# Kernel tuning notes

Measured on AMD Instinct MI355X. Metric: run time of the kernel, lower is better.

Reference implementation:

```python
import jax, jax.numpy as jnp
import numpy as np
from jax import lax

C = 64
KS = 3  # filter_ks for dynamic kernel conv


def conv2d(x, w, pad, b=None):
    out = lax.conv_general_dilated(x, w, (1, 1), [(pad, pad), (pad, pad)],
                                   dimension_numbers=("NCHW", "OIHW", "NCHW"))
    if b is not None:
        out = out + b.reshape(1, -1, 1, 1)
    return out


def kernel_conv2d(feat, kernel):
    # feat: [B,C,H,W]; kernel: [B,C*KS*KS,H,W] -> per-pixel per-channel 3x3 filter
    B, Cc, H, W = feat.shape
    pad = (KS - 1) // 2
    xp = jnp.pad(feat, ((0, 0), (0, 0), (pad, pad), (pad, pad)), mode="edge")
    # patches: [B,C,KS*KS,H,W]
    patches = jnp.stack([xp[:, :, i:i + H, j:j + W]
                         for i in range(KS) for j in range(KS)], axis=2)
    K = kernel.reshape(B, Cc, KS * KS, H, W)
    return jnp.sum(patches * K, axis=2)


def setup_inputs() -> dict:
    key = jax.random.key(0)
    ks = jax.random.split(key, 24)
    B, H, W = 8, 128, 128
    s = lambda *sh: 1.0 / np.sqrt(np.prod(sh[1:]))
    def w(k, *sh):
        return jax.random.normal(k, sh, dtype=jnp.float32) * s(*sh)
    return {
        "f_event": jax.random.normal(ks[0], (B, C, H, W), dtype=jnp.float32),
        "f_blur": jax.random.normal(ks[1], (B, C, H, W), dtype=jnp.float32),
        # trans: conv3x3 -> ReLU -> conv3x3 (no bias)
        "Wt1": w(ks[2], C, C, 3, 3), "Wt2": w(ks[3], C, C, 3, 3),
        # trans2: conv3x3 -> ReLU
        "Wt3": w(ks[4], C, C, 3, 3),
        # F_mlp: Linear(C,2C) -> ReLU -> Linear(2C,C) -> Sigmoid
        "A1": w(ks[5], 2 * C, C), "b1": jnp.zeros((2 * C,), jnp.float32),
        "A2": w(ks[6], C, 2 * C), "b2": jnp.zeros((C,), jnp.float32),
        # gernerate_kernel: conv3x3(bias) -> ReLU -> conv1x1(bias) to C*KS^2
        "G1": w(ks[7], C, C, 3, 3), "g1b": jnp.zeros((C,), jnp.float32),
        "G2": w(ks[8], C * KS * KS, C, 1, 1), "g2b": jnp.zeros((C * KS * KS,), jnp.float32),
        # gate_rgb: conv1x1 C->1, bias
        "Rw": w(ks[9], 1, C, 1, 1), "rb": jnp.zeros((1,), jnp.float32),
        # body_sa: conv3x3 -> ReLU -> conv3x3 (no bias)
        "S1": w(ks[10], C, C, 3, 3), "S2": w(ks[11], C, C, 3, 3),
        # spatial_e: BasicConv(2,1,5,pad=2,relu=False), bias
        "Ew": w(ks[12], 1, 2, 5, 5), "eb": jnp.zeros((1,), jnp.float32),
        # conv1x1_fusion: 2C->2C, no bias
        "Fw": w(ks[13], 2 * C, 2 * C, 1, 1),
    }


def reference(f_event, f_blur, Wt1, Wt2, Wt3, A1, b1, A2, b2,
              G1, g1b, G2, g2b, Rw, rb, S1, S2, Ew, eb, Fw):
    fused = f_event + f_blur
    fused = conv2d(jax.nn.relu(conv2d(fused, Wt1, 1)), Wt2, 1)  # trans
    # SE-style channel gate
    w0 = jnp.mean(fused, axis=(2, 3))                      # [B,C]
    w0 = jax.nn.relu(w0 @ A1.T + b1)
    w0 = jax.nn.sigmoid(w0 @ A2.T + b2)                    # [B,C]
    f_b = f_blur + w0[:, :, None, None] * f_blur
    fused2 = fused + jax.nn.relu(conv2d(fused, Wt3, 1))    # trans2 + residual
    rgb_att = conv2d(fused2, Rw, 0, rb)                    # [B,1,H,W]
    f_b = f_b + rgb_att * f_b
    # dynamic per-pixel kernel from events
    kern = conv2d(jax.nn.relu(conv2d(f_event, G1, 1, g1b)), G2, 0, g2b)
    f_b = f_b + kernel_conv2d(f_b, kern)
    # spatial attention on events
    sa = conv2d(jax.nn.relu(conv2d(f_event, S1, 1)), S2, 1)
    comp = jnp.concatenate([jnp.max(sa, axis=1, keepdims=True),
                            jnp.mean(sa, axis=1, keepdims=True)], axis=1)
    scale_e = jax.nn.sigmoid(conv2d(comp, Ew, 2, eb))      # [B,1,H,W]
    f_e = f_event + scale_e * f_event
    res = conv2d(jnp.concatenate([f_e, f_b], axis=1), Fw, 0)
    return res
```

## Files before the change

kernel.cpp:

```cpp
#include <hip/hip_runtime.h>
#include <math.h>

constexpr int Bn = 8, Cn = 64, Hn = 128, Wn = 128;
constexpr int HW  = Hn * Wn;
constexpr int CHW = Cn * HW;
constexpr size_t NB = (size_t)Bn * CHW;

typedef float  f32x4  __attribute__((ext_vector_type(4)));
typedef __bf16 bf16x8 __attribute__((ext_vector_type(8)));
typedef unsigned int u32x4 __attribute__((ext_vector_type(4)));
typedef unsigned int u32x2 __attribute__((ext_vector_type(2)));

static __device__ __forceinline__ unsigned short f2bf(float f) {
    unsigned u = __builtin_bit_cast(unsigned, f);
    u = (u + 0x7FFF + ((u >> 16) & 1)) >> 16;
    return (unsigned short)u;
}
static __device__ __forceinline__ float bf2f(unsigned short v) {
    unsigned u = (unsigned)v << 16;
    return __builtin_bit_cast(float, u);
}
static __device__ __forceinline__ float bfhalf(unsigned u, int hi) {
    unsigned r = hi ? (u & 0xffff0000u) : (u << 16);
    return __builtin_bit_cast(float, r);
}

static __device__ __forceinline__ void gl_lds16(const unsigned short* g, unsigned short* l) {
#if defined(__has_builtin) && __has_builtin(__builtin_amdgcn_global_load_lds)
    __builtin_amdgcn_global_load_lds(
        (const __attribute__((address_space(1))) void*)g,
        (__attribute__((address_space(3))) void*)l, 16, 0, 0);
#else
    *(u32x4*)l = *(const u32x4*)g;
#endif
}

__global__ void prep_w_k(const float* __restrict__ W0, const float* __restrict__ W1,
                         const float* __restrict__ W2, const float* __restrict__ W3,
                         const float* __restrict__ W4, const float* __restrict__ W5,
                         unsigned short* __restrict__ dst) {
    int i = blockIdx.x * 256 + threadIdx.x;
    if (i >= 36864) return;
    const float* W = W0;
    switch (blockIdx.y) {
        case 1: W = W1; break; case 2: W = W2; break;
        case 3: W = W3; break; case 4: W = W4; break; case 5: W = W5; break;
        default: break;
    }
    int cj = i & 7;
    int rest = i >> 3;
    int co = rest & 63;
    rest >>= 6;
    int t  = rest % 9;
    int hs = rest / 9;
    int ci = hs * 8 + cj;
    dst[(size_t)blockIdx.y * 36864 + i] = f2bf(W[(co * 64 + ci) * 9 + t]);
}

__global__ void prep2_k(const float* __restrict__ G2, const float* __restrict__ Fw,
                        unsigned short* __restrict__ G2p, unsigned short* __restrict__ Fwp,
                        unsigned short* __restrict__ zp) {
    int i = blockIdx.x * 256 + threadIdx.x;
    if (i < 64) zp[i] = 0;
    if (i < 36864) G2p[i] = f2bf(G2[i]);
    else if (i < 36864 + 16384) Fwp[i - 36864] = f2bf(Fw[i - 36864]);
}

__global__ void pre_blk_k(const float* __restrict__ fe, const float* __restrict__ fb,
                          unsigned short* __restrict__ evb, unsigned short* __restrict__ f0b,
                          unsigned short* __restrict__ fbb) {
    int i = blockIdx.x * 256 + threadIdx.x;
    int px = i & 16383;
    int oct = (i >> 14) & 7;
    int b = i >> 17;
    const float* pe = fe + (size_t)b * CHW + (size_t)oct * 8 * HW + px;
    const float* pb = fb + (size_t)b * CHW + (size_t)oct * 8 * HW + px;
    u32x4 ev, f0, fbv;
#pragma unroll
    for (int q = 0; q < 4; ++q) {
        float e0 = pe[(size_t)(2 * q) * HW],     b0 = pb[(size_t)(2 * q) * HW];
        float e1 = pe[(size_t)(2 * q + 1) * HW], b1 = pb[(size_t)(2 * q + 1) * HW];
        ev[q]  = (unsigned)f2bf(e0) | ((unsigned)f2bf(e1) << 16);
        f0[q]  = (unsigned)f2bf(e0 + b0) | ((unsigned)f2bf(e1 + b1) << 16);
        fbv[q] = (unsigned)f2bf(b0) | ((unsigned)f2bf(b1) << 16);
    }
    const size_t o = ((size_t)(b * 8 + oct) * HW + px) * 8;
    *(u32x4*)(evb + o) = ev;
    *(u32x4*)(f0b + o) = f0;
    *(u32x4*)(fbb + o) = fbv;
}

__global__ __launch_bounds__(256, 3) void conv3x3_l1_blk(
        const unsigned short* __restrict__ f0, const unsigned short* __restrict__ ev,
        const unsigned short* __restrict__ Wt1g, const unsigned short* __restrict__ G1g,
        const unsigned short* __restrict__ S1g, const float* __restrict__ g1b,
        unsigned short* __restrict__ out_t1, unsigned short* __restrict__ out_h,
        unsigned short* __restrict__ out_s1, const unsigned short* __restrict__ zp) {
    __shared__ unsigned short smIn[20736];
    const int z = blockIdx.z;
    const int b = z & 7, sel = z >> 3;
    const unsigned short* in = (sel == 0) ? f0 : ev;
    const unsigned short* Wg = (sel == 0) ? Wt1g : ((sel == 1) ? G1g : S1g);
    unsigned short* out = (sel == 0) ? out_t1 : ((sel == 1) ? out_h : out_s1);
    const int by = blockIdx.y << 4, bx = blockIdx.x << 4;
    const int tid = threadIdx.x;
    const int lane = tid & 63, w = tid >> 6;
    const int lx = lane & 15, ls = lane >> 4;

    for (int idx = tid; idx < 2592; idx += 256) {
        int oct = idx / 324;
        int p   = idx - oct * 324;
        int yy = p / 18, xx = p - yy * 18;
        int gy = by + yy - 1, gx = bx + xx - 1;
        const unsigned short* src =
            ((unsigned)gy < (unsigned)Hn && (unsigned)gx < (unsigned)Wn)
            ? in + ((size_t)(b * 8 + oct) * HW + gy * Wn + gx) * 8 : zp;
        gl_lds16(src, smIn + idx * 8);
    }
    __syncthreads();

    f32x4 acc[4][4];
#pragma unroll
    for (int m = 0; m < 4; ++m)
#pragma unroll
        for (int n = 0; n < 4; ++n) acc[m][n] = f32x4{0.f, 0.f, 0.f, 0.f};

#pragma unroll
    for (int ky = 0; ky < 3; ++ky)
#pragma unroll
    for (int kx = 0; kx < 3; ++kx) {
        const int t = ky * 3 + kx;
#pragma unroll
        for (int kk = 0; kk < 2; ++kk) {
            bf16x8 a[4];
            const unsigned short* wbase = Wg + kk * 18432 + ls * 4608 + t * 512 + lx * 8;
#pragma unroll
            for (int m = 0; m < 4; ++m)
                a[m] = *(const bf16x8*)(wbase + m * 128);
            const unsigned short* ibase =
                smIn + ((kk * 4 + ls) * 324 + (4 * w + ky) * 18 + lx + kx) * 8;
#pragma unroll
            for (int n = 0; n < 4; ++n) {
                bf16x8 bf = *(const bf16x8*)(ibase + n * 144);
#pragma unroll
                for (int m = 0; m < 4; ++m)
                    acc[m][n] = __builtin_amdgcn_mfma_f32_16x16x32_bf16(
                        a[m], bf, acc[m][n], 0, 0, 0);
            }
        }
    }

    const int y0 = by + 4 * w;
#pragma unroll
    for (int m = 0; m < 4; ++m) {
        float bv[4] = {0.f, 0.f, 0.f, 0.f};
        if (sel == 1) {
            float4 b4 = *(const float4*)(g1b + 16 * m + ls * 4);
            bv[0] = b4.x; bv[1] = b4.y; bv[2] = b4.z; bv[3] = b4.w;
        }
        const size_t rowb = (size_t)(b * 8 + m * 2 + (ls >> 1)) * HW;
        const int j0 = (ls & 1) * 4;
#pragma unroll
        for (int n = 0; n < 4; ++n) {
            const size_t pofs = rowb + (size_t)(y0 + n) * Wn + bx + lx;
            float vr[4];
#pragma unroll
            for (int r = 0; r < 4; ++r)
                vr[r] = fmaxf(acc[m][n][r] + bv[r], 0.f);
            u32x2 pk;
            pk[0] = (unsigned)f2bf(vr[0]) | ((unsigned)f2bf(vr[1]) << 16);
            pk[1] = (unsigned)f2bf(vr[2]) | ((unsigned)f2bf(vr[3]) << 16);
            *(u32x2*)(out + pofs * 8 + j0) = pk;
        }
    }
}

__global__ __launch_bounds__(256, 3) void conv3x3_l2_blk(
        const unsigned short* __restrict__ t1, const unsigned short* __restrict__ s1,
        const unsigned short* __restrict__ Wt2g, const unsigned short* __restrict__ S2g,
        unsigned short* __restrict__ out_f, float* __restrict__ comp,
        const unsigned short* __restrict__ zp) {
    __shared__ unsigned short smIn[20736];
    const int z = blockIdx.z;
    const int b = z & 7, sel = z >> 3;
    const unsigned short* in = (sel == 0) ? t1 : s1;
    const unsigned short* Wg = (sel == 0) ? Wt2g : S2g;
    const int by = blockIdx.y << 4, bx = blockIdx.x << 4;
    const int tid = threadIdx.x;
    const int lane = tid & 63, w = tid >> 6;
    const int lx = lane & 15, ls = lane >> 4;

    for (int idx = tid; idx < 2592; idx += 256) {
        int oct = idx / 324;
        int p   = idx - oct * 324;
        int yy = p / 18, xx = p - yy * 18;
        int gy = by + yy - 1, gx = bx + xx - 1;
        const unsigned short* src =
            ((unsigned)gy < (unsigned)Hn && (unsigned)gx < (unsigned)Wn)
            ? in + ((size_t)(b * 8 + oct) * HW + gy * Wn + gx) * 8 : zp;
        gl_lds16(src, smIn + idx * 8);
    }
    __syncthreads();

    f32x4 acc[4][4];
#pragma unroll
    for (int m = 0; m < 4; ++m)
#pragma unroll
        for (int n = 0; n < 4; ++n) acc[m][n] = f32x4{0.f, 0.f, 0.f, 0.f};

#pragma unroll
    for (int ky = 0; ky < 3; ++ky)
#pragma unroll
    for (int kx = 0; kx < 3; ++kx) {
        const int t = ky * 3 + kx;
#pragma unroll
        for (int kk = 0; kk < 2; ++kk) {
            bf16x8 a[4];
            const unsigned short* wbase = Wg + kk * 18432 + ls * 4608 + t * 512 + lx * 8;
#pragma unroll
            for (int m = 0; m < 4; ++m)
                a[m] = *(const bf16x8*)(wbase + m * 128);
            const unsigned short* ibase =
                smIn + ((kk * 4 + ls) * 324 + (4 * w + ky) * 18 + lx + kx) * 8;
#pragma unroll
            for (int n = 0; n < 4; ++n) {
                bf16x8 bf = *(const bf16x8*)(ibase + n * 144);
#pragma unroll
                for (int m = 0; m < 4; ++m)
                    acc[m][n] = __builtin_amdgcn_mfma_f32_16x16x32_bf16(
                        a[m], bf, acc[m][n], 0, 0, 0);
            }
        }
    }

    const int y0 = by + 4 * w;
    if (sel == 0) {
#pragma unroll
        for (int m = 0; m < 4; ++m) {
            const size_t rowb = (size_t)(b * 8 + m * 2 + (ls >> 1)) * HW;
            const int j0 = (ls & 1) * 4;
#pragma unroll
            for (int n = 0; n < 4; ++n) {
                const size_t pofs = rowb + (size_t)(y0 + n) * Wn + bx + lx;
                u32x2 pk;
                pk[0] = (unsigned)f2bf(acc[m][n][0]) | ((unsigned)f2bf(acc[m][n][1]) << 16);
                pk[1] = (unsigned)f2bf(acc[m][n][2]) | ((unsigned)f2bf(acc[m][n][3]) << 16);
                *(u32x2*)(out_f + pofs * 8 + j0) = pk;
            }
        }
    } else {
        float gs[4], gm[4];
#pragma unroll
        for (int n = 0; n < 4; ++n) { gs[n] = 0.f; gm[n] = -1e30f; }
#pragma unroll
        for (int m = 0; m < 4; ++m)
#pragma unroll
            for (int r = 0; r < 4; ++r)
#pragma unroll
                for (int n = 0; n < 4; ++n) {
                    float v = acc[m][n][r];
                    gm[n] = fmaxf(gm[n], v);
                    gs[n] += v;
                }
#pragma unroll
        for (int n = 0; n < 4; ++n) {
            float s = gs[n], mx = gm[n];
            s += __shfl_xor(s, 16);
            s += __shfl_xor(s, 32);
            mx = fmaxf(mx, __shfl_xor(mx, 16));
            mx = fmaxf(mx, __shfl_xor(mx, 32));
            if (ls == 0) {
                const size_t o = (size_t)b * 2 * HW + (size_t)(y0 + n) * Wn + bx + lx;
                comp[o]      = mx;
                comp[o + HW] = s * (1.f / 64.f);
            }
        }
    }
}

__global__ __launch_bounds__(256, 3) void rgb_sconv_k(
        const unsigned short* __restrict__ in, const unsigned short* __restrict__ Wg,
        const float* __restrict__ gw, const float* __restrict__ gb,
        float* __restrict__ gout,
        const float* __restrict__ comp, const float* __restrict__ Ew,
        const float* __restrict__ eb, float* __restrict__ scale,
        const unsigned short* __restrict__ zp) {
    __shared__ unsigned short smIn[20736];
    const int z = blockIdx.z;
    if (z >= 8) {
        int id = (((z - 8) * 64) + blockIdx.y * 8 + blockIdx.x) * 256 + threadIdx.x;
        int sb = id >> 14, p = id & 16383;
        int y = p >> 7, x = p & 127;
        const float* cb = comp + (size_t)sb * 2 * HW;
        float sacc = eb[0];
#pragma unroll
        for (int ch = 0; ch < 2; ++ch)
#pragma unroll
            for (int ky = 0; ky < 5; ++ky) {
                int gy = y + ky - 2;
                if ((unsigned)gy >= (unsigned)Hn) continue;
#pragma unroll
                for (int kx = 0; kx < 5; ++kx) {
                    int gx = x + kx - 2;
                    if ((unsigned)gx >= (unsigned)Wn) continue;
                    sacc = fmaf(Ew[ch * 25 + ky * 5 + kx], cb[ch * HW + gy * Wn + gx], sacc);
                }
            }
        scale[id] = 1.f / (1.f + expf(-sacc));
        return;
    }
    const int b = z;
    const int by = blockIdx.y << 4, bx = blockIdx.x << 4;
    const int tid = threadIdx.x;
    const int lane = tid & 63, w = tid >> 6;
    const int lx = lane & 15, ls = lane >> 4;

    for (int idx = tid; idx < 2592; idx += 256) {
        int oct = idx / 324;
        int p   = idx - oct * 324;
        int yy = p / 18, xx = p - yy * 18;
        int gy = by + yy - 1, gx = bx + xx - 1;
        const unsigned short* src =
            ((unsigned)gy < (unsigned)Hn && (unsigned)gx < (unsigned)Wn)
            ? in + ((size_t)(b * 8 + oct) * HW + gy * Wn + gx) * 8 : zp;
        gl_lds16(src, smIn + idx * 8);
    }
    __syncthreads();

    f32x4 acc[4][4];
#pragma unroll
    for (int m = 0; m < 4; ++m)
#pragma unroll
        for (int n = 0; n < 4; ++n) acc[m][n] = f32x4{0.f, 0.f, 0.f, 0.f};

#pragma unroll
    for (int ky = 0; ky < 3; ++ky)
#pragma unroll
    for (int kx = 0; kx < 3; ++kx) {
        const int t = ky * 3 + kx;
#pragma unroll
        for (int kk = 0; kk < 2; ++kk) {
            bf16x8 a[4];
            const unsigned short* wbase = Wg + kk * 18432 + ls * 4608 + t * 512 + lx * 8;
#pragma unroll
            for (int m = 0; m < 4; ++m)
                a[m] = *(const bf16x8*)(wbase + m * 128);
            const unsigned short* ibase =
                smIn + ((kk * 4 + ls) * 324 + (4 * w + ky) * 18 + lx + kx) * 8;
#pragma unroll
            for (int n = 0; n < 4; ++n) {
                bf16x8 bf = *(const bf16x8*)(ibase + n * 144);
#pragma unroll
                for (int m = 0; m < 4; ++m)
                    acc[m][n] = __builtin_amdgcn_mfma_f32_16x16x32_bf16(
                        a[m], bf, acc[m][n], 0, 0, 0);
            }
        }
    }

    const int y0 = by + 4 * w;
    float gs[4];
#pragma unroll
    for (int n = 0; n < 4; ++n) gs[n] = 0.f;
#pragma unroll
    for (int m = 0; m < 4; ++m) {
        float4 rw4 = *(const float4*)(gw + 16 * m + ls * 4);
        const float rwf[4] = {rw4.x, rw4.y, rw4.z, rw4.w};
        const size_t rowb = (size_t)(b * 8 + m * 2 + (ls >> 1)) * HW;
        const int j0 = (ls & 1) * 4;
#pragma unroll
        for (int n = 0; n < 4; ++n) {
            const size_t pofs = rowb + (size_t)(y0 + n) * Wn + bx + lx;
            u32x2 rin = *(const u32x2*)(in + pofs * 8 + j0);
#pragma unroll
            for (int r = 0; r < 4; ++r) {
                float v = fmaxf(acc[m][n][r], 0.f) + bfhalf(rin[r >> 1], r & 1);
                gs[n] = fmaf(rwf[r], v, gs[n]);
            }
        }
    }
#pragma unroll
    for (int n = 0; n < 4; ++n) {
        float s = gs[n];
        s += __shfl_xor(s, 16);
        s += __shfl_xor(s, 32);
        if (ls == 0)
            gout[(size_t)b * HW + (size_t)(y0 + n) * Wn + bx + lx] = s + gb[0];
    }
}

__global__ void mean_hw_blk(const unsigned short* __restrict__ in, float* __restrict__ w0) {
    __shared__ float red[256][8];
    const int bo = blockIdx.x;
    const int tid = threadIdx.x;
    const unsigned short* p = in + (size_t)bo * HW * 8;
    float s[8];
#pragma unroll
    for (int j = 0; j < 8; ++j) s[j] = 0.f;
    for (int it = 0; it < 64; ++it) {
        u32x4 v = *(const u32x4*)(p + (size_t)(tid + it * 256) * 8);
#pragma unroll
        for (int j = 0; j < 8; ++j) s[j] += bfhalf(v[j >> 1], j & 1);
    }
#pragma unroll
    for (int j = 0; j < 8; ++j) red[tid][j] = s[j];
    __syncthreads();
    for (int off = 128; off > 0; off >>= 1) {
        if (tid < off)
#pragma unroll
            for (int j = 0; j < 8; ++j) red[tid][j] += red[tid + off][j];
        __syncthreads();
    }
    if (tid < 8) w0[bo * 8 + tid] = red[0][tid] * (1.f / 16384.f);
}

__global__ void mlp_k(const float* __restrict__ w0, const float* __restrict__ A1,
                      const float* __restrict__ b1, const float* __restrict__ A2,
                      const float* __restrict__ b2, float* __restrict__ w0s) {
    int b = blockIdx.x, t = threadIdx.x;
    __shared__ float w0r[64], hid[128];
    if (t < 64) w0r[t] = w0[b * 64 + t];
    __syncthreads();
    float s = b1[t];
    for (int c = 0; c < 64; ++c) s = fmaf(A1[t * 64 + c], w0r[c], s);
    hid[t] = fmaxf(s, 0.f);
    __syncthreads();
    if (t < 64) {
        float s2 = b2[t];
        for (int j = 0; j < 128; ++j) s2 = fmaf(A2[t * 128 + j], hid[j], s2);
        w0s[b * 64 + t] = 1.f / (1.f + expf(-s2));
    }
}

__global__ __launch_bounds__(256, 4) void dynfused_k(
        const unsigned short* __restrict__ fbb, const unsigned short* __restrict__ hb,
        const unsigned short* __restrict__ G2p, const float* __restrict__ g2b,
        const float* __restrict__ w0s, const float* __restrict__ rgb,
        unsigned short* __restrict__ outb) {
    __shared__ unsigned short smU[8192];
    __shared__ unsigned short smFB[11520];
    const int b  = blockIdx.z;
    const int by = blockIdx.y << 3, bx = blockIdx.x << 4;
    const int tid = threadIdx.x;
    const int lane = tid & 63, w = tid >> 6;
    const int lx = lane & 15, ls = lane >> 4;
    const int wr = w & 1, wc = w >> 1;
    const int px = tid & 127;
    const int chalf = __builtin_amdgcn_readfirstlane(tid >> 7);
    const int ty = px >> 4, tx = px & 15;

#pragma unroll
    for (int it = 0; it < 4; ++it) {
        int i = tid + it * 256;
        int p = i & 127, oct = i >> 7;
        gl_lds16(hb + ((size_t)(b * 8 + oct) * HW + (by + (p >> 4)) * Wn + bx + (p & 15)) * 8,
                 smU + i * 8);
    }
    const float* rgbb = rgb + (size_t)b * HW;
    for (int i = tid; i < 1440; i += 256) {
        int oct = i / 180, p = i - oct * 180;
        int pr = p / 18, pc = p - pr * 18;
        int gy = min(max(by + pr - 1, 0), Hn - 1);
        int gx = min(max(bx + pc - 1, 0), Wn - 1);
        u32x4 v = *(const u32x4*)(fbb + ((size_t)(b * 8 + oct) * HW + gy * Wn + gx) * 8);
        float g = 1.f + rgbb[gy * Wn + gx];
        float4 s0 = *(const float4*)(w0s + b * 64 + oct * 8);
        float4 s1 = *(const float4*)(w0s + b * 64 + oct * 8 + 4);
        const float sc[8] = {1.f + s0.x, 1.f + s0.y, 1.f + s0.z, 1.f + s0.w,
                             1.f + s1.x, 1.f + s1.y, 1.f + s1.z, 1.f + s1.w};
#pragma unroll
        for (int j = 0; j < 8; ++j)
            smFB[(oct * 8 + j) * 180 + p] = f2bf(bfhalf(v[j >> 1], j & 1) * sc[j] * g);
    }
    __syncthreads();

    bf16x8 bv[2][4];
#pragma unroll
    for (int kk = 0; kk < 2; ++kk)
#pragma unroll
        for (int n = 0; n < 4; ++n)
            bv[kk][n] = *(const bf16x8*)(smU + ((kk * 4 + ls) * 128 + wc * 64 + n * 16 + lx) * 8);
    __syncthreads();

    float acc[32];
#pragma unroll
    for (int s = 0; s < 32; ++s) acc[s] = 0.f;

#pragma unroll
    for (int chunk = 0; chunk < 9; ++chunk) {
        f32x4 ka[2][4];
#pragma unroll
        for (int m = 0; m < 2; ++m)
#pragma unroll
            for (int n = 0; n < 4; ++n) ka[m][n] = f32x4{0.f, 0.f, 0.f, 0.f};
#pragma unroll
        for (int kk = 0; kk < 2; ++kk) {
            bf16x8 a[2];
#pragma unroll
            for (int m = 0; m < 2; ++m)
                a[m] = *(const bf16x8*)(G2p +
                        (size_t)(chunk * 64 + wr * 32 + m * 16 + lx) * 64 + kk * 32 + ls * 8);
#pragma unroll
            for (int n = 0; n < 4; ++n)
#pragma unroll
                for (int m = 0; m < 2; ++m)
                    ka[m][n] = __builtin_amdgcn_mfma_f32_16x16x32_bf16(a[m], bv[kk][n], ka[m][n], 0, 0, 0);
        }
#pragma unroll
        for (int m = 0; m < 2; ++m) {
            const float4 bb4 = *(const float4*)(g2b + chunk * 64 + wr * 32 + m * 16 + ls * 4);
            const float bb[4] = {bb4.x, bb4.y, bb4.z, bb4.w};
            const int rl0 = wr * 32 + m * 16 + ls * 4;
            const int gr = rl0 >> 3, sub = rl0 & 7;
#pragma unroll
            for (int n = 0; n < 4; ++n) {
                const int pxl = wc * 64 + n * 16 + lx;
                u32x2 pk;
                pk[0] = (unsigned)f2bf(ka[m][n][0] + bb[0]) |
                        ((unsigned)f2bf(ka[m][n][1] + bb[1]) << 16);
                pk[1] = (unsigned)f2bf(ka[m][n][2] + bb[2]) |
                        ((unsigned)f2bf(ka[m][n][3] + bb[3]) << 16);
                *(u32x2*)(smU + pxl * 64 + ((gr ^ (pxl & 7)) << 3) + sub) = pk;
            }
        }
        __syncthreads();
        u32x4 kvr[8];
#pragma unroll
        for (int k = 0; k < 8; ++k)
            kvr[k] = *(const u32x4*)(smU + px * 64 + ((k ^ (px & 7)) << 3));
#pragma unroll
        for (int rl = 0; rl < 64; ++rl) {
            const int r = chunk * 64 + rl;
            const int c = r / 9, t = r - c * 9;
            const int s = c >> 1;
            if ((c & 1) == chalf) {
                float kv = bfhalf(kvr[rl >> 3][(rl & 7) >> 1], rl & 1);
                float pv = bf2f(smFB[c * 180 + (ty + t / 3) * 18 + tx + (t % 3)]);
                acc[s] = fmaf(kv, pv, acc[s]);
            }
        }
        __syncthreads();
    }

#pragma unroll
    for (int s = 0; s < 32; ++s) {
        const int c = 2 * s + chalf;
        float res = bf2f(smFB[c * 180 + (ty + 1) * 18 + (tx + 1)]);
        smU[c * 128 + px] = f2bf(acc[s] + res);
    }
    __syncthreads();
#pragma unroll
    for (int it = 0; it < 4; ++it) {
        int i = tid + it * 256;
        int p = i & 127, oct = i >> 7;
        u32x4 pk;
#pragma unroll
        for (int q = 0; q < 4; ++q)
            pk[q] = (unsigned)smU[(oct * 8 + 2 * q) * 128 + p] |
                    ((unsigned)smU[(oct * 8 + 2 * q + 1) * 128 + p] << 16);
        *(u32x4*)(outb + ((size_t)(b * 8 + oct) * HW + (by + (p >> 4)) * Wn + bx + (p & 15)) * 8) = pk;
    }
}

__global__ __launch_bounds__(256, 3) void fuse_mfma_k(
        const unsigned short* __restrict__ evb, const float* __restrict__ scale,
        const unsigned short* __restrict__ fb2b, const unsigned short* __restrict__ Fwp,
        float* __restrict__ out) {
    __shared__ unsigned short smF[16384];
    const int bid = blockIdx.x;
    const int b = bid >> 7, px0 = (bid & 127) << 7;
    const int tid = threadIdx.x;
    const int lane = tid & 63, w = tid >> 6;
    const int lx = lane & 15, ls = lane >> 4;
    const int wr = w & 1, wc = w >> 1;
    const float* sc = scale + b * HW + px0;

#pragma unroll
    for (int it = 4; it < 8; ++it) {
        int slot = tid + it * 256;
        int oct = slot >> 7, pxl = slot & 127;
        gl_lds16(fb2b + ((size_t)(b * 8 + oct - 8) * HW + px0 + pxl) * 8, smF + slot * 8);
    }
#pragma unroll
    for (int it = 0; it < 4; ++it) {
        int slot = tid + it * 256;
        int oct = slot >> 7, pxl = slot & 127;
        u32x4 v = *(const u32x4*)(evb + ((size_t)(b * 8 + oct) * HW + px0 + pxl) * 8);
        float s = 1.f + sc[pxl];
#pragma unroll
        for (int q = 0; q < 4; ++q)
            v[q] = (unsigned)f2bf(bfhalf(v[q], 0) * s) |
                   ((unsigned)f2bf(bfhalf(v[q], 1) * s) << 16);
        ((u32x4*)smF)[slot] = v;
    }
    __syncthreads();

    f32x4 acc[4][4];
#pragma unroll
    for (int m = 0; m < 4; ++m)
#pragma unroll
        for (int n = 0; n < 4; ++n) acc[m][n] = f32x4{0.f, 0.f, 0.f, 0.f};

#pragma unroll
    for (int kk = 0; kk < 4; ++kk) {
        bf16x8 a[4];
#pragma unroll
        for (int m = 0; m < 4; ++m)
            a[m] = *(const bf16x8*)(Fwp + (size_t)(wr * 64 + m * 16 + lx) * 128 + kk * 32 + ls * 8);
#pragma unroll
        for (int n = 0; n < 4; ++n) {
            bf16x8 bv = *(const bf16x8*)(smF + ((kk * 4 + ls) * 128 + wc * 64 + n * 16 + lx) * 8);
#pragma unroll
            for (int m = 0; m < 4; ++m)
                acc[m][n] = __builtin_amdgcn_mfma_f32_16x16x32_bf16(a[m], bv, acc[m][n], 0, 0, 0);
        }
    }

    const size_t ob = (size_t)b * 2 * CHW + px0 + wc * 64;
#pragma unroll
    for (int m = 0; m < 4; ++m)
#pragma unroll
        for (int n = 0; n < 4; ++n)
#pragma unroll
            for (int j = 0; j < 4; ++j) {
                const int co = wr * 64 + m * 16 + ls * 4 + j;
                out[ob + (size_t)co * HW + n * 16 + lx] = acc[m][n][j];
            }
}

extern "C" void kernel_launch(void* const* d_in, const int* in_sizes, int n_in,
                              void* d_out, int out_size, void* d_ws, size_t ws_size,
                              hipStream_t stream) {
    const float* f_event = (const float*)d_in[0];
    const float* f_blur  = (const float*)d_in[1];
    const float* Wt1 = (const float*)d_in[2];
    const float* Wt2 = (const float*)d_in[3];
    const float* Wt3 = (const float*)d_in[4];
    const float* A1  = (const float*)d_in[5];
    const float* b1  = (const float*)d_in[6];
    const float* A2  = (const float*)d_in[7];
    const float* b2  = (const float*)d_in[8];
    const float* G1  = (const float*)d_in[9];
    const float* g1b = (const float*)d_in[10];
    const float* G2  = (const float*)d_in[11];
    const float* g2b = (const float*)d_in[12];
    const float* Rw  = (const float*)d_in[13];
    const float* rb  = (const float*)d_in[14];
    const float* S1  = (const float*)d_in[15];
    const float* S2  = (const float*)d_in[16];
    const float* Ew  = (const float*)d_in[17];
    const float* eb  = (const float*)d_in[18];
    const float* Fw  = (const float*)d_in[19];
    float* out = (float*)d_out;

    float* ws    = (float*)d_ws;
    float* w0    = ws;
    float* w0s   = w0 + 512;
    float* rgb   = w0s + 512;
    float* comp  = rgb + Bn * HW;
    float* scale = comp + 2 * Bn * HW;
    unsigned short* wprep = (unsigned short*)(scale + Bn * HW);
    unsigned short* G2p = wprep + 6 * 36864;
    unsigned short* Fwp = G2p + 36864;
    unsigned short* zpad = Fwp + 16384;
    unsigned short* B0 = zpad + 64;
    unsigned short* B1 = B0 + NB;
    unsigned short* B2 = B1 + NB;
    unsigned short* B3 = B2 + NB;
    unsigned short* B4 = B3 + NB;
    unsigned short* B5 = B4 + NB;
    unsigned short* B6 = B5 + NB;

    prep_w_k<<<dim3(144, 6), 256, 0, stream>>>(Wt1, Wt2, Wt3, G1, S1, S2, wprep);
    prep2_k<<<208, 256, 0, stream>>>(G2, Fw, G2p, Fwp, zpad);
    pre_blk_k<<<4096, 256, 0, stream>>>(f_event, f_blur, B0, B1, B5);
    conv3x3_l1_blk<<<dim3(8, 8, 24), 256, 0, stream>>>(
        B1, B0, wprep + 0 * 36864, wprep + 3 * 36864, wprep + 4 * 36864, g1b,
        B2, B4, B6, zpad);
    conv3x3_l2_blk<<<dim3(8, 8, 16), 256, 0, stream>>>(
        B2, B6, wprep + 1 * 36864, wprep + 5 * 36864, B3, comp, zpad);
    mean_hw_blk<<<Bn * 8, 256, 0, stream>>>(B3, w0);
    mlp_k<<<Bn, 128, 0, stream>>>(w0, A1, b1, A2, b2, w0s);
    rgb_sconv_k<<<dim3(8, 8, 16), 256, 0, stream>>>(
        B3, wprep + 2 * 36864, Rw, rb, rgb, comp, Ew, eb, scale, zpad);
    dynfused_k<<<dim3(8, 16, Bn), 256, 0, stream>>>(B5, B4, G2p, g2b, w0s, rgb, B3);
    fuse_mfma_k<<<Bn * HW / 128, 256, 0, stream>>>(B0, scale, B3, Fwp, out);
}
```

Before: 220.8 us.

## Fuse event+blur sum into conv load, spatial mean into conv epilogue

Stops writing the bf16 f_event+f_blur buffer in the pre-pass and instead forms the sum while staging the halo tile in the first conv. It also drops the separate mean-over-HW kernel by reducing the trans conv output per tile with wave shuffles and float atomics into a zeroed w0 buffer, with the 1/HW scale moved into the MLP. The rgb conv reads its residual from the already-staged shared tile rather than global memory. This saves one full-tensor write and read plus one launch, at the cost of register-path loads for sel 0 in conv1 and nondeterministic atomic summation order.

```diff
diff --git a/kernel.cpp b/kernel.cpp
--- a/kernel.cpp
+++ b/kernel.cpp
@@ -59,39 +59,37 @@
 
 __global__ void prep2_k(const float* __restrict__ G2, const float* __restrict__ Fw,
                         unsigned short* __restrict__ G2p, unsigned short* __restrict__ Fwp,
-                        unsigned short* __restrict__ zp) {
+                        unsigned short* __restrict__ zp, float* __restrict__ w0z) {
     int i = blockIdx.x * 256 + threadIdx.x;
     if (i < 64) zp[i] = 0;
+    if (i < 512) w0z[i] = 0.f;
     if (i < 36864) G2p[i] = f2bf(G2[i]);
     else if (i < 36864 + 16384) Fwp[i - 36864] = f2bf(Fw[i - 36864]);
 }
 
 __global__ void pre_blk_k(const float* __restrict__ fe, const float* __restrict__ fb,
-                          unsigned short* __restrict__ evb, unsigned short* __restrict__ f0b,
-                          unsigned short* __restrict__ fbb) {
+                          unsigned short* __restrict__ evb, unsigned short* __restrict__ fbb) {
     int i = blockIdx.x * 256 + threadIdx.x;
     int px = i & 16383;
     int oct = (i >> 14) & 7;
     int b = i >> 17;
     const float* pe = fe + (size_t)b * CHW + (size_t)oct * 8 * HW + px;
     const float* pb = fb + (size_t)b * CHW + (size_t)oct * 8 * HW + px;
-    u32x4 ev, f0, fbv;
+    u32x4 ev, fbv;
 #pragma unroll
     for (int q = 0; q < 4; ++q) {
         float e0 = pe[(size_t)(2 * q) * HW],     b0 = pb[(size_t)(2 * q) * HW];
         float e1 = pe[(size_t)(2 * q + 1) * HW], b1 = pb[(size_t)(2 * q + 1) * HW];
         ev[q]  = (unsigned)f2bf(e0) | ((unsigned)f2bf(e1) << 16);
-        f0[q]  = (unsigned)f2bf(e0 + b0) | ((unsigned)f2bf(e1 + b1) << 16);
         fbv[q] = (unsigned)f2bf(b0) | ((unsigned)f2bf(b1) << 16);
     }
     const size_t o = ((size_t)(b * 8 + oct) * HW + px) * 8;
     *(u32x4*)(evb + o) = ev;
-    *(u32x4*)(f0b + o) = f0;
     *(u32x4*)(fbb + o) = fbv;
 }
 
 __global__ __launch_bounds__(256, 3) void conv3x3_l1_blk(
-        const unsigned short* __restrict__ f0, const unsigned short* __restrict__ ev,
+        const unsigned short* __restrict__ evb, const unsigned short* __restrict__ fbb,
         const unsigned short* __restrict__ Wt1g, const unsigned short* __restrict__ G1g,
         const unsigned short* __restrict__ S1g, const float* __restrict__ g1b,
         unsigned short* __restrict__ out_t1, unsigned short* __restrict__ out_h,
@@ -99,9 +97,103 @@
     __shared__ unsigned short smIn[20736];
     const int z = blockIdx.z;
     const int b = z & 7, sel = z >> 3;
-    const unsigned short* in = (sel == 0) ? f0 : ev;
     const unsigned short* Wg = (sel == 0) ? Wt1g : ((sel == 1) ? G1g : S1g);
     unsigned short* out = (sel == 0) ? out_t1 : ((sel == 1) ? out_h : out_s1);
+    const int by = blockIdx.y << 4, bx = blockIdx.x << 4;
+    const int tid = threadIdx.x;
+    const int lane = tid & 63, w = tid >> 6;
+    const int lx = lane & 15, ls = lane >> 4;
+
+    for (int idx = tid; idx < 2592; idx += 256) {
+        int oct = idx / 324;
+        int p   = idx - oct * 324;
+        int yy = p / 18, xx = p - yy * 18;
+        int gy = by + yy - 1, gx = bx + xx - 1;
+        bool ok = (unsigned)gy < (unsigned)Hn && (unsigned)gx < (unsigned)Wn;
+        const size_t off = ((size_t)(b * 8 + oct) * HW + gy * Wn + gx) * 8;
+        if (sel == 0) {
+            u32x4 v = u32x4{0u, 0u, 0u, 0u};
+            if (ok) {
+                u32x4 e = *(const u32x4*)(evb + off);
+                u32x4 f = *(const u32x4*)(fbb + off);
+#pragma unroll
+                for (int q = 0; q < 4; ++q)
+                    v[q] = (unsigned)f2bf(bfhalf(e[q], 0) + bfhalf(f[q], 0)) |
+                           ((unsigned)f2bf(bfhalf(e[q], 1) + bfhalf(f[q], 1)) << 16);
+            }
+            *(u32x4*)(smIn + idx * 8) = v;
+        } else {
+            gl_lds16(ok ? evb + off : zp, smIn + idx * 8);
+        }
+    }
+    __syncthreads();
+
+    f32x4 acc[4][4];
+#pragma unroll
+    for (int m = 0; m < 4; ++m)
+#pragma unroll
+        for (int n = 0; n < 4; ++n) acc[m][n] = f32x4{0.f, 0.f, 0.f, 0.f};
+
+#pragma unroll
+    for (int ky = 0; ky < 3; ++ky)
+#pragma unroll
+    for (int kx = 0; kx < 3; ++kx) {
+        const int t = ky * 3 + kx;
+#pragma unroll
+        for (int kk = 0; kk < 2; ++kk) {
+            bf16x8 a[4];
+            const unsigned short* wbase = Wg + kk * 18432 + ls * 4608 + t * 512 + lx * 8;
+#pragma unroll
+            for (int m = 0; m < 4; ++m)
+                a[m] = *(const bf16x8*)(wbase + m * 128);
+            const unsigned short* ibase =
+                smIn + ((kk * 4 + ls) * 324 + (4 * w + ky) * 18 + lx + kx) * 8;
+#pragma unroll
+            for (int n = 0; n < 4; ++n) {
+                bf16x8 bf = *(const bf16x8*)(ibase + n * 144);
+#pragma unroll
+                for (int m = 0; m < 4; ++m)
+                    acc[m][n] = __builtin_amdgcn_mfma_f32_16x16x32_bf16(
+                        a[m], bf, acc[m][n], 0, 0, 0);
+            }
+        }
+    }
+
+    const int y0 = by + 4 * w;
+#pragma unroll
+    for (int m = 0; m < 4; ++m) {
+        float bv[4] = {0.f, 0.f, 0.f, 0.f};
+        if (sel == 1) {
+            float4 b4 = *(const float4*)(g1b + 16 * m + ls * 4);
+            bv[0] = b4.x; bv[1] = b4.y; bv[2] = b4.z; bv[3] = b4.w;
+        }
+        const size_t rowb = (size_t)(b * 8 + m * 2 + (ls >> 1)) * HW;
+        const int j0 = (ls & 1) * 4;
+#pragma unroll
+        for (int n = 0; n < 4; ++n) {
+            const size_t pofs = rowb + (size_t)(y0 + n) * Wn + bx + lx;
+            float vr[4];
+#pragma unroll
+            for (int r = 0; r < 4; ++r)
+                vr[r] = fmaxf(acc[m][n][r] + bv[r], 0.f);
+            u32x2 pk;
+            pk[0] = (unsigned)f2bf(vr[0]) | ((unsigned)f2bf(vr[1]) << 16);
+            pk[1] = (unsigned)f2bf(vr[2]) | ((unsigned)f2bf(vr[3]) << 16);
+            *(u32x2*)(out + pofs * 8 + j0) = pk;
+        }
+    }
+}
+
+__global__ __launch_bounds__(256, 3) void conv3x3_l2_blk(
+        const unsigned short* __restrict__ t1, const unsigned short* __restrict__ s1,
+        const unsigned short* __restrict__ Wt2g, const unsigned short* __restrict__ S2g,
+        unsigned short* __restrict__ out_f, float* __restrict__ comp,
+        float* __restrict__ w0, const unsigned short* __restrict__ zp) {
+    __shared__ unsigned short smIn[20736];
+    const int z = blockIdx.z;
+    const int b = z & 7, sel = z >> 3;
+    const unsigned short* in = (sel == 0) ? t1 : s1;
+    const unsigned short* Wg = (sel == 0) ? Wt2g : S2g;
     const int by = blockIdx.y << 4, bx = blockIdx.x << 4;
     const int tid = threadIdx.x;
     const int lane = tid & 63, w = tid >> 6;
@@ -151,89 +243,6 @@
     }
 
     const int y0 = by + 4 * w;
-#pragma unroll
-    for (int m = 0; m < 4; ++m) {
-        float bv[4] = {0.f, 0.f, 0.f, 0.f};
-        if (sel == 1) {
-            float4 b4 = *(const float4*)(g1b + 16 * m + ls * 4);
-            bv[0] = b4.x; bv[1] = b4.y; bv[2] = b4.z; bv[3] = b4.w;
-        }
-        const size_t rowb = (size_t)(b * 8 + m * 2 + (ls >> 1)) * HW;
-        const int j0 = (ls & 1) * 4;
-#pragma unroll
-        for (int n = 0; n < 4; ++n) {
-            const size_t pofs = rowb + (size_t)(y0 + n) * Wn + bx + lx;
-            float vr[4];
-#pragma unroll
-            for (int r = 0; r < 4; ++r)
-                vr[r] = fmaxf(acc[m][n][r] + bv[r], 0.f);
-            u32x2 pk;
-            pk[0] = (unsigned)f2bf(vr[0]) | ((unsigned)f2bf(vr[1]) << 16);
-            pk[1] = (unsigned)f2bf(vr[2]) | ((unsigned)f2bf(vr[3]) << 16);
-            *(u32x2*)(out + pofs * 8 + j0) = pk;
-        }
-    }
-}
-
-__global__ __launch_bounds__(256, 3) void conv3x3_l2_blk(
-        const unsigned short* __restrict__ t1, const unsigned short* __restrict__ s1,
-        const unsigned short* __restrict__ Wt2g, const unsigned short* __restrict__ S2g,
-        unsigned short* __restrict__ out_f, float* __restrict__ comp,
-        const unsigned short* __restrict__ zp) {
-    __shared__ unsigned short smIn[20736];
-    const int z = blockIdx.z;
-    const int b = z & 7, sel = z >> 3;
-    const unsigned short* in = (sel == 0) ? t1 : s1;
-    const unsigned short* Wg = (sel == 0) ? Wt2g : S2g;
-    const int by = blockIdx.y << 4, bx = blockIdx.x << 4;
-    const int tid = threadIdx.x;
-    const int lane = tid & 63, w = tid >> 6;
-    const int lx = lane & 15, ls = lane >> 4;
-
-    for (int idx = tid; idx < 2592; idx += 256) {
-        int oct = idx / 324;
-        int p   = idx - oct * 324;
-        int yy = p / 18, xx = p - yy * 18;
-        int gy = by + yy - 1, gx = bx + xx - 1;
-        const unsigned short* src =
-            ((unsigned)gy < (unsigned)Hn && (unsigned)gx < (unsigned)Wn)
-            ? in + ((size_t)(b * 8 + oct) * HW + gy * Wn + gx) * 8 : zp;
-        gl_lds16(src, smIn + idx * 8);
-    }
-    __syncthreads();
-
-    f32x4 acc[4][4];
-#pragma unroll
-    for (int m = 0; m < 4; ++m)
-#pragma unroll
-        for (int n = 0; n < 4; ++n) acc[m][n] = f32x4{0.f, 0.f, 0.f, 0.f};
-
-#pragma unroll
-    for (int ky = 0; ky < 3; ++ky)
-#pragma unroll
-    for (int kx = 0; kx < 3; ++kx) {
-        const int t = ky * 3 + kx;
-#pragma unroll
-        for (int kk = 0; kk < 2; ++kk) {
-            bf16x8 a[4];
-            const unsigned short* wbase = Wg + kk * 18432 + ls * 4608 + t * 512 + lx * 8;
-#pragma unroll
-            for (int m = 0; m < 4; ++m)
-                a[m] = *(const bf16x8*)(wbase + m * 128);
-            const unsigned short* ibase =
-                smIn + ((kk * 4 + ls) * 324 + (4 * w + ky) * 18 + lx + kx) * 8;
-#pragma unroll
-            for (int n = 0; n < 4; ++n) {
-                bf16x8 bf = *(const bf16x8*)(ibase + n * 144);
-#pragma unroll
-                for (int m = 0; m < 4; ++m)
-                    acc[m][n] = __builtin_amdgcn_mfma_f32_16x16x32_bf16(
-                        a[m], bf, acc[m][n], 0, 0, 0);
-            }
-        }
-    }
-
-    const int y0 = by + 4 * w;
     if (sel == 0) {
 #pragma unroll
         for (int m = 0; m < 4; ++m) {
@@ -246,6 +255,16 @@
                 pk[0] = (unsigned)f2bf(acc[m][n][0]) | ((unsigned)f2bf(acc[m][n][1]) << 16);
                 pk[1] = (unsigned)f2bf(acc[m][n][2]) | ((unsigned)f2bf(acc[m][n][3]) << 16);
                 *(u32x2*)(out_f + pofs * 8 + j0) = pk;
+            }
+#pragma unroll
+            for (int r = 0; r < 4; ++r) {
+                float s = acc[m][0][r] + acc[m][1][r] + acc[m][2][r] + acc[m][3][r];
+                s += __shfl_xor(s, 1);
+                s += __shfl_xor(s, 2);
+                s += __shfl_xor(s, 4);
+                s += __shfl_xor(s, 8);
+                if (lx == 0)
+                    atomicAdd(&w0[b * 64 + 16 * m + ls * 4 + r], s);
             }
         }
     } else {
@@ -366,12 +385,12 @@
     for (int m = 0; m < 4; ++m) {
         float4 rw4 = *(const float4*)(gw + 16 * m + ls * 4);
         const float rwf[4] = {rw4.x, rw4.y, rw4.z, rw4.w};
-        const size_t rowb = (size_t)(b * 8 + m * 2 + (ls >> 1)) * HW;
+        const int oct = m * 2 + (ls >> 1);
         const int j0 = (ls & 1) * 4;
 #pragma unroll
         for (int n = 0; n < 4; ++n) {
-            const size_t pofs = rowb + (size_t)(y0 + n) * Wn + bx + lx;
-            u32x2 rin = *(const u32x2*)(in + pofs * 8 + j0);
+            u32x2 rin = *(const u32x2*)(smIn +
+                (oct * 324 + (4 * w + n + 1) * 18 + lx + 1) * 8 + j0);
 #pragma unroll
             for (int r = 0; r < 4; ++r) {
                 float v = fmaxf(acc[m][n][r], 0.f) + bfhalf(rin[r >> 1], r & 1);
@@ -389,37 +408,12 @@
     }
 }
 
-__global__ void mean_hw_blk(const unsigned short* __restrict__ in, float* __restrict__ w0) {
-    __shared__ float red[256][8];
-    const int bo = blockIdx.x;
-    const int tid = threadIdx.x;
-    const unsigned short* p = in + (size_t)bo * HW * 8;
-    float s[8];
-#pragma unroll
-    for (int j = 0; j < 8; ++j) s[j] = 0.f;
-    for (int it = 0; it < 64; ++it) {
-        u32x4 v = *(const u32x4*)(p + (size_t)(tid + it * 256) * 8);
-#pragma unroll
-        for (int j = 0; j < 8; ++j) s[j] += bfhalf(v[j >> 1], j & 1);
-    }
-#pragma unroll
-    for (int j = 0; j < 8; ++j) red[tid][j] = s[j];
-    __syncthreads();
-    for (int off = 128; off > 0; off >>= 1) {
-        if (tid < off)
-#pragma unroll
-            for (int j = 0; j < 8; ++j) red[tid][j] += red[tid + off][j];
-        __syncthreads();
-    }
-    if (tid < 8) w0[bo * 8 + tid] = red[0][tid] * (1.f / 16384.f);
-}
-
 __global__ void mlp_k(const float* __restrict__ w0, const float* __restrict__ A1,
                       const float* __restrict__ b1, const float* __restrict__ A2,
                       const float* __restrict__ b2, float* __restrict__ w0s) {
     int b = blockIdx.x, t = threadIdx.x;
     __shared__ float w0r[64], hid[128];
-    if (t < 64) w0r[t] = w0[b * 64 + t];
+    if (t < 64) w0r[t] = w0[b * 64 + t] * (1.f / 16384.f);
     __syncthreads();
     float s = b1[t];
     for (int c = 0; c < 64; ++c) s = fmaf(A1[t * 64 + c], w0r[c], s);
@@ -664,22 +658,20 @@
     unsigned short* Fwp = G2p + 36864;
     unsigned short* zpad = Fwp + 16384;
     unsigned short* B0 = zpad + 64;
-    unsigned short* B1 = B0 + NB;
-    unsigned short* B2 = B1 + NB;
+    unsigned short* B2 = B0 + NB;
     unsigned short* B3 = B2 + NB;
     unsigned short* B4 = B3 + NB;
     unsigned short* B5 = B4 + NB;
     unsigned short* B6 = B5 + NB;
 
     prep_w_k<<<dim3(144, 6), 256, 0, stream>>>(Wt1, Wt2, Wt3, G1, S1, S2, wprep);
-    prep2_k<<<208, 256, 0, stream>>>(G2, Fw, G2p, Fwp, zpad);
-    pre_blk_k<<<4096, 256, 0, stream>>>(f_event, f_blur, B0, B1, B5);
+    prep2_k<<<208, 256, 0, stream>>>(G2, Fw, G2p, Fwp, zpad, w0);
+    pre_blk_k<<<4096, 256, 0, stream>>>(f_event, f_blur, B0, B5);
     conv3x3_l1_blk<<<dim3(8, 8, 24), 256, 0, stream>>>(
-        B1, B0, wprep + 0 * 36864, wprep + 3 * 36864, wprep + 4 * 36864, g1b,
+        B0, B5, wprep + 0 * 36864, wprep + 3 * 36864, wprep + 4 * 36864, g1b,
         B2, B4, B6, zpad);
     conv3x3_l2_blk<<<dim3(8, 8, 16), 256, 0, stream>>>(
-        B2, B6, wprep + 1 * 36864, wprep + 5 * 36864, B3, comp, zpad);
-    mean_hw_blk<<<Bn * 8, 256, 0, stream>>>(B3, w0);
+        B2, B6, wprep + 1 * 36864, wprep + 5 * 36864, B3, comp, w0, zpad);
     mlp_k<<<Bn, 128, 0, stream>>>(w0, A1, b1, A2, b2, w0s);
     rgb_sconv_k<<<dim3(8, 8, 16), 256, 0, stream>>>(
         B3, wprep + 2 * 36864, Rw, rb, rgb, comp, Ew, eb, scale, zpad);
```

New measurement: 232.3 us. 1.05x slower.

## Fuse final 1x1 fusion conv into dynamic-kernel conv kernel

Applied to the files above, without the earlier changes.

Merges the final 1x1 fusion conv (MFMA GEMM over concatenated scaled-event and f_b features) into the dynamic per-pixel kernel-conv kernel. The f_b result stays in LDS instead of being written to global memory and read back by a separate launch, and the shared buffers are merged into one region to hold the concatenated tile. The output store now uses 2D tile (8x16) addressing, which makes global writes less contiguous, and the larger fused kernel may see higher register and LDS pressure.

```diff
diff --git a/kernel.cpp b/kernel.cpp
--- a/kernel.cpp
+++ b/kernel.cpp
@@ -436,9 +436,11 @@
         const unsigned short* __restrict__ fbb, const unsigned short* __restrict__ hb,
         const unsigned short* __restrict__ G2p, const float* __restrict__ g2b,
         const float* __restrict__ w0s, const float* __restrict__ rgb,
-        unsigned short* __restrict__ outb) {
-    __shared__ unsigned short smU[8192];
-    __shared__ unsigned short smFB[11520];
+        const unsigned short* __restrict__ evb, const float* __restrict__ scale,
+        const unsigned short* __restrict__ Fwp, float* __restrict__ out) {
+    __shared__ __align__(16) unsigned short smA[19712];
+    unsigned short* smU  = smA;
+    unsigned short* smFB = smA + 8192;
     const int b  = blockIdx.z;
     const int by = blockIdx.y << 3, bx = blockIdx.x << 4;
     const int tid = threadIdx.x;
@@ -528,6 +530,7 @@
 #pragma unroll
         for (int k = 0; k < 8; ++k)
             kvr[k] = *(const u32x4*)(smU + px * 64 + ((k ^ (px & 7)) << 3));
+        __syncthreads();
 #pragma unroll
         for (int rl = 0; rl < 64; ++rl) {
             const int r = chunk * 64 + rl;
@@ -539,93 +542,70 @@
                 acc[s] = fmaf(kv, pv, acc[s]);
             }
         }
-        __syncthreads();
     }
 
 #pragma unroll
     for (int s = 0; s < 32; ++s) {
         const int c = 2 * s + chalf;
-        float res = bf2f(smFB[c * 180 + (ty + 1) * 18 + (tx + 1)]);
-        smU[c * 128 + px] = f2bf(acc[s] + res);
-    }
-    __syncthreads();
+        acc[s] += bf2f(smFB[c * 180 + (ty + 1) * 18 + (tx + 1)]);
+    }
+    __syncthreads();
+#pragma unroll
+    for (int s = 0; s < 32; ++s) {
+        const int c = 2 * s + chalf;
+        smA[((8 + (c >> 3)) * 128 + px) * 8 + (c & 7)] = f2bf(acc[s]);
+    }
 #pragma unroll
     for (int it = 0; it < 4; ++it) {
         int i = tid + it * 256;
         int p = i & 127, oct = i >> 7;
-        u32x4 pk;
+        int gy = by + (p >> 4), gx = bx + (p & 15);
+        u32x4 v = *(const u32x4*)(evb + ((size_t)(b * 8 + oct) * HW + gy * Wn + gx) * 8);
+        float sv = 1.f + scale[(size_t)b * HW + gy * Wn + gx];
 #pragma unroll
         for (int q = 0; q < 4; ++q)
-            pk[q] = (unsigned)smU[(oct * 8 + 2 * q) * 128 + p] |
-                    ((unsigned)smU[(oct * 8 + 2 * q + 1) * 128 + p] << 16);
-        *(u32x4*)(outb + ((size_t)(b * 8 + oct) * HW + (by + (p >> 4)) * Wn + bx + (p & 15)) * 8) = pk;
-    }
-}
-
-__global__ __launch_bounds__(256, 3) void fuse_mfma_k(
-        const unsigned short* __restrict__ evb, const float* __restrict__ scale,
-        const unsigned short* __restrict__ fb2b, const unsigned short* __restrict__ Fwp,
-        float* __restrict__ out) {
-    __shared__ unsigned short smF[16384];
-    const int bid = blockIdx.x;
-    const int b = bid >> 7, px0 = (bid & 127) << 7;
-    const int tid = threadIdx.x;
-    const int lane = tid & 63, w = tid >> 6;
-    const int lx = lane & 15, ls = lane >> 4;
-    const int wr = w & 1, wc = w >> 1;
-    const float* sc = scale + b * HW + px0;
-
-#pragma unroll
-    for (int it = 4; it < 8; ++it) {
-        int slot = tid + it * 256;
-        int oct = slot >> 7, pxl = slot & 127;
-        gl_lds16(fb2b + ((size_t)(b * 8 + oct - 8) * HW + px0 + pxl) * 8, smF + slot * 8);
-    }
-#pragma unroll
-    for (int it = 0; it < 4; ++it) {
-        int slot = tid + it * 256;
-        int oct = slot >> 7, pxl = slot & 127;
-        u32x4 v = *(const u32x4*)(evb + ((size_t)(b * 8 + oct) * HW + px0 + pxl) * 8);
-        float s = 1.f + sc[pxl];
-#pragma unroll
-        for (int q = 0; q < 4; ++q)
-            v[q] = (unsigned)f2bf(bfhalf(v[q], 0) * s) |
-                   ((unsigned)f2bf(bfhalf(v[q], 1) * s) << 16);
-        ((u32x4*)smF)[slot] = v;
-    }
-    __syncthreads();
-
-    f32x4 acc[4][4];
-#pragma unroll
-    for (int m = 0; m < 4; ++m)
-#pragma unroll
-        for (int n = 0; n < 4; ++n) acc[m][n] = f32x4{0.f, 0.f, 0.f, 0.f};
-
-#pragma unroll
-    for (int kk = 0; kk < 4; ++kk) {
-        bf16x8 a[4];
-#pragma unroll
-        for (int m = 0; m < 4; ++m)
-            a[m] = *(const bf16x8*)(Fwp + (size_t)(wr * 64 + m * 16 + lx) * 128 + kk * 32 + ls * 8);
-#pragma unroll
-        for (int n = 0; n < 4; ++n) {
-            bf16x8 bv = *(const bf16x8*)(smF + ((kk * 4 + ls) * 128 + wc * 64 + n * 16 + lx) * 8);
-#pragma unroll
-            for (int m = 0; m < 4; ++m)
-                acc[m][n] = __builtin_amdgcn_mfma_f32_16x16x32_bf16(a[m], bv, acc[m][n], 0, 0, 0);
-        }
-    }
-
-    const size_t ob = (size_t)b * 2 * CHW + px0 + wc * 64;
-#pragma unroll
-    for (int m = 0; m < 4; ++m)
-#pragma unroll
-        for (int n = 0; n < 4; ++n)
-#pragma unroll
-            for (int j = 0; j < 4; ++j) {
-                const int co = wr * 64 + m * 16 + ls * 4 + j;
-                out[ob + (size_t)co * HW + n * 16 + lx] = acc[m][n][j];
-            }
+            v[q] = (unsigned)f2bf(bfhalf(v[q], 0) * sv) |
+                   ((unsigned)f2bf(bfhalf(v[q], 1) * sv) << 16);
+        *(u32x4*)(smA + (oct * 128 + p) * 8) = v;
+    }
+    __syncthreads();
+
+    const size_t ob = (size_t)b * 2 * CHW;
+#pragma unroll
+    for (int mh = 0; mh < 2; ++mh) {
+        f32x4 a2[2][4];
+#pragma unroll
+        for (int m = 0; m < 2; ++m)
+#pragma unroll
+            for (int n = 0; n < 4; ++n) a2[m][n] = f32x4{0.f, 0.f, 0.f, 0.f};
+#pragma unroll
+        for (int kk = 0; kk < 4; ++kk) {
+            bf16x8 af[2];
+#pragma unroll
+            for (int m = 0; m < 2; ++m)
+                af[m] = *(const bf16x8*)(Fwp +
+                        (size_t)(wr * 64 + mh * 32 + m * 16 + lx) * 128 + kk * 32 + ls * 8);
+#pragma unroll
+            for (int n = 0; n < 4; ++n) {
+                bf16x8 bvv = *(const bf16x8*)(smA + ((kk * 4 + ls) * 128 + wc * 64 + n * 16 + lx) * 8);
+#pragma unroll
+                for (int m = 0; m < 2; ++m)
+                    a2[m][n] = __builtin_amdgcn_mfma_f32_16x16x32_bf16(af[m], bvv, a2[m][n], 0, 0, 0);
+            }
+        }
+#pragma unroll
+        for (int m = 0; m < 2; ++m)
+#pragma unroll
+            for (int n = 0; n < 4; ++n) {
+                const int pxl = wc * 64 + n * 16 + lx;
+                const int gy = by + (pxl >> 4), gx = bx + (pxl & 15);
+#pragma unroll
+                for (int j = 0; j < 4; ++j) {
+                    const int co = wr * 64 + mh * 32 + m * 16 + ls * 4 + j;
+                    out[ob + (size_t)co * HW + (size_t)gy * Wn + gx] = a2[m][n][j];
+                }
+            }
+    }
 }
 
 extern "C" void kernel_launch(void* const* d_in, const int* in_sizes, int n_in,
@@ -683,6 +663,6 @@
     mlp_k<<<Bn, 128, 0, stream>>>(w0, A1, b1, A2, b2, w0s);
     rgb_sconv_k<<<dim3(8, 8, 16), 256, 0, stream>>>(
         B3, wprep + 2 * 36864, Rw, rb, rgb, comp, Ew, eb, scale, zpad);
-    dynfused_k<<<dim3(8, 16, Bn), 256, 0, stream>>>(B5, B4, G2p, g2b, w0s, rgb, B3);
-    fuse_mfma_k<<<Bn * HW / 128, 256, 0, stream>>>(B0, scale, B3, Fwp, out);
-}
+    dynfused_k<<<dim3(8, 16, Bn), 256, 0, stream>>>(
+        B5, B4, G2p, g2b, w0s, rgb, B0, scale, Fwp, out);
+}
```

Measured after the change: 208.6 us. 1.06x faster.
